# Kernel tuning notes

Hardware: AMD Instinct MI355X
Metric: run time of the kernel (lower is better)

Reference implementation:

```python
import jax, jax.numpy as jnp
import numpy as np

H = 256       # hidden_dim
E = H // 2    # operator embedding dim
T = 12        # num_tempers
O = 3         # num_ops per temper
HOPS = 4      # max_path_hops
B = 128       # batch
D = 2048      # input_dim
NCLS = 10     # task_head classes


def setup_inputs() -> dict:
    key = jax.random.key(0)
    ks = jax.random.split(key, 12)
    x = jax.random.normal(ks[0], (B, D), jnp.float32)
    N = B * (D // H)  # 1024 patch tokens
    # per-hop routed temper per patch; value == T means halt
    sampled_tempers = jax.random.randint(ks[1], (HOPS, N), 0, T + 1, jnp.int32)
    sampled_ops = jax.random.randint(ks[2], (HOPS, N), 0, O, jnp.int32)
    s1 = 1.0 / np.sqrt(H + E)
    W1 = jax.random.uniform(ks[3], (T, O, H + E, H), jnp.float32, -s1, s1)
    b1 = jax.random.uniform(ks[4], (T, O, H), jnp.float32, -s1, s1)
    s2 = 1.0 / np.sqrt(H)
    W2 = jax.random.uniform(ks[5], (T, O, H, H), jnp.float32, -s2, s2)
    b2 = jax.random.uniform(ks[6], (T, O, H), jnp.float32, -s2, s2)
    op_emb = jax.random.normal(ks[7], (T, O, E), jnp.float32)
    ln_g = jnp.ones((H,), jnp.float32)
    ln_b = jnp.zeros((H,), jnp.float32)
    Wt = jax.random.uniform(ks[8], (H, NCLS), jnp.float32, -s2, s2)
    bt = jax.random.uniform(ks[9], (NCLS,), jnp.float32, -s2, s2)
    return dict(x=x, W1=W1, b1=b1, W2=W2, b2=b2, op_emb=op_emb,
                ln_g=ln_g, ln_b=ln_b, Wt=Wt, bt=bt,
                sampled_tempers=sampled_tempers, sampled_ops=sampled_ops)


def reference(x, W1, b1, W2, b2, op_emb, ln_g, ln_b, Wt, bt,
              sampled_tempers, sampled_ops):
    Bsz, Din = x.shape
    pad = (-Din) % H
    if pad > 0:
        x = jnp.pad(x, ((0, 0), (0, pad)))
    state = x.reshape(-1, H)                       # [N, H] patch states
    active = jnp.ones((state.shape[0],), bool)     # not-yet-halted mask
    for hop in range(HOPS):
        t = sampled_tempers[hop]
        o = sampled_ops[hop]
        active = active & (t != T)                 # T == halt action
        tc = jnp.clip(t, 0, T - 1)                 # safe index for halted rows
        emb = op_emb[tc, o]                        # [N, E] op embedding gather
        xa = jnp.concatenate([state, emb], axis=-1)  # [N, H+E]
        # per-token expert weight gather + batched matvec (memory-bound dispatch)
        h = jax.nn.relu(jnp.einsum('ni,nio->no', xa, W1[tc, o]) + b1[tc, o])
        y = jax.nn.relu(jnp.einsum('ni,nio->no', h, W2[tc, o]) + b2[tc, o])
        state = jnp.where(active[:, None], y, state)
    pooled = state.reshape(Bsz, -1, H).mean(axis=1)   # [B, H]
    mu = pooled.mean(axis=-1, keepdims=True)
    var = pooled.var(axis=-1, keepdims=True)
    normed = (pooled - mu) * jax.lax.rsqrt(var + 1e-5) * ln_g + ln_b
    return normed @ Wt + bt                           # [B, 10]
```

## Files before the change

kernel.cpp:

```cpp
#include <hip/hip_runtime.h>

typedef __attribute__((ext_vector_type(8))) short short8;
typedef __attribute__((ext_vector_type(4))) float floatx4;

#define NEXP   36
#define NTOK   1024
#define HOPS   4

#define OFF_STATE   0u
#define OFF_W1B     1048576u
#define OFF_W2B     5767168u
#define OFF_C1      10485760u
#define OFF_COUNTS  10522624u
#define OFF_LISTS   10523264u
#define OFF_JOBS    11113088u
#define OFF_NJ      11115136u

__device__ __forceinline__ unsigned short f2bf(float f) {
    unsigned u = __float_as_uint(f);
    u += 0x7FFFu + ((u >> 16) & 1u);
    return (unsigned short)(u >> 16);
}

__global__ __launch_bounds__(256) void prep_kernel(
    const float* __restrict__ W1, const float* __restrict__ b1,
    const float* __restrict__ W2, const float* __restrict__ op_emb,
    const int* __restrict__ tempers, const int* __restrict__ ops,
    unsigned short* __restrict__ W1b, unsigned short* __restrict__ W2b,
    float* __restrict__ c1, int* __restrict__ counts, int* __restrict__ lists,
    int* __restrict__ jobs, int* __restrict__ njobs)
{
    const int bid = blockIdx.x;
    const int t = threadIdx.x;

    if (bid == 0) {
        __shared__ int lc[HOPS * NEXP];
        if (t < HOPS * NEXP) lc[t] = 0;
        __syncthreads();
        for (int q = 0; q < 4; q++) {
            int n = q * 256 + t;
            bool act = true;
            for (int hop = 0; hop < HOPS; hop++) {
                int tt = tempers[hop * NTOK + n];
                int oo = ops[hop * NTOK + n];
                act = act && (tt != 12);
                if (act) {
                    int e = tt * 3 + oo;
                    int pos = atomicAdd(&lc[hop * NEXP + e], 1);
                    lists[(hop * NEXP + e) * NTOK + pos] = n;
                }
            }
        }
        __syncthreads();
        if (t < HOPS * NEXP) counts[t] = lc[t];
        if (t < HOPS) {
            int hop = t, nj = 0;
            for (int e = 0; e < NEXP; e++) {
                int c = lc[hop * NEXP + e];
                for (int m0 = 0; m0 < c; m0 += 16)
                    jobs[hop * 128 + nj++] = (m0 << 8) | e;
            }
            njobs[hop] = nj;
        }
    } else if (bid <= 2304) {
        const int id0 = bid - 1;
        const int mat = id0 / 1152;
        const int id  = id0 % 1152;
        const int e   = id / 32;
        const int sub = id % 32;
        const int kb  = sub / 4;
        const int jt  = sub % 4;
        const float* src = mat ? (W2 + e * 65536) : (W1 + e * 98304);
        unsigned short* dst = (mat ? W2b : W1b) + e * 65536;
        const int j  = jt * 64 + (t & 63);
        const int ks = (t >> 6) * 8;
        short8 v;
        #pragma unroll
        for (int i = 0; i < 8; i++)
            v[i] = (short)f2bf(src[(kb * 32 + ks + i) * 256 + j]);
        *(short8*)(dst + (kb * 256 + j) * 32 + ks) = v;
    } else {
        const int e = bid - 2305;
        __shared__ float eb[128];
        if (t < 128) eb[t] = op_emb[e * 128 + t];
        __syncthreads();
        float acc = b1[e * 256 + t];
        const float* wp = W1 + e * 98304 + 256 * 256;
        #pragma unroll 4
        for (int k = 0; k < 128; k++)
            acc += eb[k] * wp[k * 256 + t];
        c1[e * 256 + t] = acc;
    }
}

__global__ __launch_bounds__(1024, 4) void hop_kernel(
    const float* __restrict__ src, float* __restrict__ state,
    const unsigned short* __restrict__ W1b,
    const unsigned short* __restrict__ W2b,
    const float* __restrict__ c1, const float* __restrict__ b2,
    const int* __restrict__ counts, const int* __restrict__ lists,
    const int* __restrict__ jobs, const int* __restrict__ njobs, int hop)
{
    if (blockIdx.x >= njobs[hop]) return;
    const int job = jobs[hop * 128 + blockIdx.x];
    const int e   = job & 0xFF;
    const int m0  = job >> 8;
    const int n_e = counts[hop * NEXP + e];
    const int mact = min(16, n_e - m0);

    const int t = threadIdx.x;
    const int l = t & 63, w = t >> 6;
    const int col = l & 15, g = l >> 4;
    const int j = w * 16 + col;

    const unsigned short* Wp  = W1b + e * 65536;
    const unsigned short* Wp2 = W2b + e * 65536;
    short8 B1[8], B2[8];
    #pragma unroll
    for (int kb = 0; kb < 8; kb++) {
        B1[kb] = *(const short8*)(Wp  + (kb * 256 + j) * 32 + g * 8);
        B2[kb] = *(const short8*)(Wp2 + (kb * 256 + j) * 32 + g * 8);
    }
    #pragma unroll
    for (int kb = 0; kb < 8; kb++) {
        int4 p1 = __builtin_bit_cast(int4, B1[kb]);
        int4 p2 = __builtin_bit_cast(int4, B2[kb]);
        asm volatile("" : "+v"(p1.x), "+v"(p1.y), "+v"(p1.z), "+v"(p1.w),
                          "+v"(p2.x), "+v"(p2.y), "+v"(p2.z), "+v"(p2.w));
        B1[kb] = __builtin_bit_cast(short8, p1);
        B2[kb] = __builtin_bit_cast(short8, p2);
    }
    const float cv = c1[e * 256 + j];
    const float bv = b2[e * 256 + j];

    __shared__ int toks[16];
    __shared__ unsigned short Ab[4096];
    __shared__ unsigned short Hb[4096];

    if (t < 16) toks[t] = (t < mact) ? lists[(hop * NEXP + e) * NTOK + m0 + t] : 0;
    __syncthreads();

    {
        int m = t >> 6;
        int k = (t & 63) * 4;
        float4 v = make_float4(0.f, 0.f, 0.f, 0.f);
        if (m < mact) v = *(const float4*)(src + toks[m] * 256 + k);
        int kb = k >> 5, gg = (k >> 3) & 3, i = k & 7;
        unsigned short* d = Ab + kb * 512 + (gg * 16 + m) * 8 + i;
        d[0] = f2bf(v.x); d[1] = f2bf(v.y); d[2] = f2bf(v.z); d[3] = f2bf(v.w);
    }
    __syncthreads();

    floatx4 acc = (floatx4){cv, cv, cv, cv};
    #pragma unroll
    for (int kb = 0; kb < 8; kb++) {
        short8 a = *(const short8*)(Ab + kb * 512 + l * 8);
        acc = __builtin_amdgcn_mfma_f32_16x16x32_bf16(a, B1[kb], acc, 0, 0, 0);
    }
    {
        int kb2 = j >> 5, g2 = (j >> 3) & 3, i2 = j & 7;
        #pragma unroll
        for (int r = 0; r < 4; r++) {
            int m = g * 4 + r;
            float vv = acc[r];
            vv = vv > 0.f ? vv : 0.f;
            Hb[kb2 * 512 + (g2 * 16 + m) * 8 + i2] = f2bf(vv);
        }
    }
    __syncthreads();

    floatx4 acc2 = (floatx4){bv, bv, bv, bv};
    #pragma unroll
    for (int kb = 0; kb < 8; kb++) {
        short8 a = *(const short8*)(Hb + kb * 512 + l * 8);
        acc2 = __builtin_amdgcn_mfma_f32_16x16x32_bf16(a, B2[kb], acc2, 0, 0, 0);
    }
    #pragma unroll
    for (int r = 0; r < 4; r++) {
        int m = g * 4 + r;
        if (m < mact) {
            float vv = acc2[r];
            state[toks[m] * 256 + j] = vv > 0.f ? vv : 0.f;
        }
    }
}

__global__ __launch_bounds__(256) void final_kernel(
    const float* __restrict__ x, const float* __restrict__ state,
    const int* __restrict__ tempers,
    const float* __restrict__ ln_g, const float* __restrict__ ln_b,
    const float* __restrict__ Wt, const float* __restrict__ bt,
    float* __restrict__ out)
{
    const int b = blockIdx.x, t = threadIdx.x;
    float s = 0.f;
    #pragma unroll
    for (int p = 0; p < 8; p++) {
        int n = b * 8 + p;
        const float* rowsrc = (tempers[n] != 12) ? state : x;
        s += rowsrc[n * 256 + t];
    }
    s *= 0.125f;

    float v1 = s, v2 = s * s;
    #pragma unroll
    for (int off = 32; off; off >>= 1) {
        v1 += __shfl_down(v1, off);
        v2 += __shfl_down(v2, off);
    }
    __shared__ float red[8];
    __shared__ float stats[2];
    const int w = t >> 6, l = t & 63;
    if (l == 0) { red[w] = v1; red[4 + w] = v2; }
    __syncthreads();
    if (t == 0) {
        float su = red[0] + red[1] + red[2] + red[3];
        float sq = red[4] + red[5] + red[6] + red[7];
        float mu = su * (1.0f / 256.0f);
        float var = sq * (1.0f / 256.0f) - mu * mu;
        stats[0] = mu;
        stats[1] = rsqrtf(var + 1e-5f);
    }
    __syncthreads();
    float normed = (s - stats[0]) * stats[1] * ln_g[t] + ln_b[t];

    __shared__ float pr[40];
    #pragma unroll
    for (int c = 0; c < 10; c++) {
        float pv = normed * Wt[t * 10 + c];
        #pragma unroll
        for (int off = 32; off; off >>= 1) pv += __shfl_down(pv, off);
        if (l == 0) pr[w * 10 + c] = pv;
    }
    __syncthreads();
    if (t < 10)
        out[b * 10 + t] = pr[t] + pr[10 + t] + pr[20 + t] + pr[30 + t] + bt[t];
}

extern "C" void kernel_launch(void* const* d_in, const int* in_sizes, int n_in,
                              void* d_out, int out_size, void* d_ws, size_t ws_size,
                              hipStream_t stream)
{
    const float* x      = (const float*)d_in[0];
    const float* W1     = (const float*)d_in[1];
    const float* b1     = (const float*)d_in[2];
    const float* W2     = (const float*)d_in[3];
    const float* b2     = (const float*)d_in[4];
    const float* op_emb = (const float*)d_in[5];
    const float* ln_g   = (const float*)d_in[6];
    const float* ln_b   = (const float*)d_in[7];
    const float* Wt     = (const float*)d_in[8];
    const float* bt     = (const float*)d_in[9];
    const int* tempers  = (const int*)d_in[10];
    const int* ops      = (const int*)d_in[11];

    char* ws = (char*)d_ws;
    float* state          = (float*)(ws + OFF_STATE);
    unsigned short* W1b   = (unsigned short*)(ws + OFF_W1B);
    unsigned short* W2b   = (unsigned short*)(ws + OFF_W2B);
    float* c1             = (float*)(ws + OFF_C1);
    int* counts           = (int*)(ws + OFF_COUNTS);
    int* lists            = (int*)(ws + OFF_LISTS);
    int* jobs             = (int*)(ws + OFF_JOBS);
    int* njobs            = (int*)(ws + OFF_NJ);
    float* out            = (float*)d_out;

    prep_kernel<<<2341, 256, 0, stream>>>(W1, b1, W2, op_emb, tempers, ops,
                                          W1b, W2b, c1, counts, lists,
                                          jobs, njobs);
    for (int hop = 0; hop < HOPS; hop++)
        hop_kernel<<<100, 1024, 0, stream>>>(hop == 0 ? x : state, state,
                                             W1b, W2b, c1, b2,
                                             counts, lists, jobs, njobs, hop);
    final_kernel<<<128, 256, 0, stream>>>(x, state, tempers,
                                          ln_g, ln_b, Wt, bt, out);
}
```

Before: 144.3 us.

## Convert fp32 expert weights to bf16 inside hop kernel instead of prepass

Removes the prep-stage pass that converted all 36 experts' W1/W2 into a blocked bf16 workspace layout. Each hop block now reads its expert's fp32 weights directly, with strided per-element loads, and rounds them to bf16 in registers. This avoids writing and re-reading about 9 MB of converted weights for experts that may be used only a few times. In exchange, each hop job reads twice the bytes through uncoalesced scalar loads, repeated across the 4 hops and multiple jobs per expert.

```diff
diff --git a/kernel.cpp b/kernel.cpp
--- a/kernel.cpp
+++ b/kernel.cpp
@@ -8,13 +8,11 @@
 #define HOPS   4
 
 #define OFF_STATE   0u
-#define OFF_W1B     1048576u
-#define OFF_W2B     5767168u
-#define OFF_C1      10485760u
-#define OFF_COUNTS  10522624u
-#define OFF_LISTS   10523264u
-#define OFF_JOBS    11113088u
-#define OFF_NJ      11115136u
+#define OFF_C1      1048576u
+#define OFF_COUNTS  1085440u
+#define OFF_LISTS   1086016u
+#define OFF_JOBS    1675840u
+#define OFF_NJ      1677888u
 
 __device__ __forceinline__ unsigned short f2bf(float f) {
     unsigned u = __float_as_uint(f);
@@ -24,16 +22,26 @@
 
 __global__ __launch_bounds__(256) void prep_kernel(
     const float* __restrict__ W1, const float* __restrict__ b1,
-    const float* __restrict__ W2, const float* __restrict__ op_emb,
+    const float* __restrict__ op_emb,
     const int* __restrict__ tempers, const int* __restrict__ ops,
-    unsigned short* __restrict__ W1b, unsigned short* __restrict__ W2b,
     float* __restrict__ c1, int* __restrict__ counts, int* __restrict__ lists,
     int* __restrict__ jobs, int* __restrict__ njobs)
 {
     const int bid = blockIdx.x;
     const int t = threadIdx.x;
 
-    if (bid == 0) {
+    if (bid < 36) {
+        const int e = bid;
+        __shared__ float eb[128];
+        if (t < 128) eb[t] = op_emb[e * 128 + t];
+        __syncthreads();
+        float acc = b1[e * 256 + t];
+        const float* wp = W1 + e * 98304 + 256 * 256;
+        #pragma unroll 4
+        for (int k = 0; k < 128; k++)
+            acc += eb[k] * wp[k * 256 + t];
+        c1[e * 256 + t] = acc;
+    } else {
         __shared__ int lc[HOPS * NEXP];
         if (t < HOPS * NEXP) lc[t] = 0;
         __syncthreads();
@@ -62,41 +70,12 @@
             }
             njobs[hop] = nj;
         }
-    } else if (bid <= 2304) {
-        const int id0 = bid - 1;
-        const int mat = id0 / 1152;
-        const int id  = id0 % 1152;
-        const int e   = id / 32;
-        const int sub = id % 32;
-        const int kb  = sub / 4;
-        const int jt  = sub % 4;
-        const float* src = mat ? (W2 + e * 65536) : (W1 + e * 98304);
-        unsigned short* dst = (mat ? W2b : W1b) + e * 65536;
-        const int j  = jt * 64 + (t & 63);
-        const int ks = (t >> 6) * 8;
-        short8 v;
-        #pragma unroll
-        for (int i = 0; i < 8; i++)
-            v[i] = (short)f2bf(src[(kb * 32 + ks + i) * 256 + j]);
-        *(short8*)(dst + (kb * 256 + j) * 32 + ks) = v;
-    } else {
-        const int e = bid - 2305;
-        __shared__ float eb[128];
-        if (t < 128) eb[t] = op_emb[e * 128 + t];
-        __syncthreads();
-        float acc = b1[e * 256 + t];
-        const float* wp = W1 + e * 98304 + 256 * 256;
-        #pragma unroll 4
-        for (int k = 0; k < 128; k++)
-            acc += eb[k] * wp[k * 256 + t];
-        c1[e * 256 + t] = acc;
     }
 }
 
 __global__ __launch_bounds__(1024, 4) void hop_kernel(
     const float* __restrict__ src, float* __restrict__ state,
-    const unsigned short* __restrict__ W1b,
-    const unsigned short* __restrict__ W2b,
+    const float* __restrict__ W1, const float* __restrict__ W2,
     const float* __restrict__ c1, const float* __restrict__ b2,
     const int* __restrict__ counts, const int* __restrict__ lists,
     const int* __restrict__ jobs, const int* __restrict__ njobs, int hop)
@@ -113,13 +92,26 @@
     const int col = l & 15, g = l >> 4;
     const int j = w * 16 + col;
 
-    const unsigned short* Wp  = W1b + e * 65536;
-    const unsigned short* Wp2 = W2b + e * 65536;
+    const float* Wp  = W1 + e * 98304;
+    const float* Wp2 = W2 + e * 65536;
     short8 B1[8], B2[8];
     #pragma unroll
     for (int kb = 0; kb < 8; kb++) {
-        B1[kb] = *(const short8*)(Wp  + (kb * 256 + j) * 32 + g * 8);
-        B2[kb] = *(const short8*)(Wp2 + (kb * 256 + j) * 32 + g * 8);
+        float v1[8], v2[8];
+        #pragma unroll
+        for (int i = 0; i < 8; i++) {
+            int k = kb * 32 + g * 8 + i;
+            v1[i] = Wp [k * 256 + j];
+            v2[i] = Wp2[k * 256 + j];
+        }
+        short8 b1v, b2v;
+        #pragma unroll
+        for (int i = 0; i < 8; i++) {
+            b1v[i] = (short)f2bf(v1[i]);
+            b2v[i] = (short)f2bf(v2[i]);
+        }
+        B1[kb] = b1v;
+        B2[kb] = b2v;
     }
     #pragma unroll
     for (int kb = 0; kb < 8; kb++) {
@@ -256,8 +248,6 @@
 
     char* ws = (char*)d_ws;
     float* state          = (float*)(ws + OFF_STATE);
-    unsigned short* W1b   = (unsigned short*)(ws + OFF_W1B);
-    unsigned short* W2b   = (unsigned short*)(ws + OFF_W2B);
     float* c1             = (float*)(ws + OFF_C1);
     int* counts           = (int*)(ws + OFF_COUNTS);
     int* lists            = (int*)(ws + OFF_LISTS);
@@ -265,12 +255,11 @@
     int* njobs            = (int*)(ws + OFF_NJ);
     float* out            = (float*)d_out;
 
-    prep_kernel<<<2341, 256, 0, stream>>>(W1, b1, W2, op_emb, tempers, ops,
-                                          W1b, W2b, c1, counts, lists,
-                                          jobs, njobs);
+    prep_kernel<<<37, 256, 0, stream>>>(W1, b1, op_emb, tempers, ops,
+                                        c1, counts, lists, jobs, njobs);
     for (int hop = 0; hop < HOPS; hop++)
         hop_kernel<<<100, 1024, 0, stream>>>(hop == 0 ? x : state, state,
-                                             W1b, W2b, c1, b2,
+                                             W1, W2, c1, b2,
                                              counts, lists, jobs, njobs, hop);
     final_kernel<<<128, 256, 0, stream>>>(x, state, tempers,
                                           ln_g, ln_b, Wt, bt, out);
```

New measurement: 156.4 us. 1.08x slower.
